# Kernel tuning notes

Hardware: AMD Instinct MI355X
Metric: run time of the kernel (lower is better)

The kernel has to match this reference:

```python
import jax, jax.numpy as jnp
import numpy as np

B, L, H = 2, 2048, 2048
NH, KVH = 16, 4
D = H // NH          # 128
G = NH // KVH        # 4 query heads per kv head
LN_EPS = 1e-12


def setup_inputs() -> dict:
    key = jax.random.key(0)
    ks = jax.random.split(key, 6)
    s = 0.02
    return {
        "hidden_state": jax.random.normal(ks[0], (B, L, H), jnp.float32),
        "mask": jnp.zeros((B, 1, 1, L), jnp.float32),
        "Wq": jax.random.normal(ks[1], (H, H), jnp.float32) * s,
        "bq": jnp.zeros((H,), jnp.float32),
        "Wk": jax.random.normal(ks[2], (KVH * D, H), jnp.float32) * s,
        "bk": jnp.zeros((KVH * D,), jnp.float32),
        "Wv": jax.random.normal(ks[3], (KVH * D, H), jnp.float32) * s,
        "bv": jnp.zeros((KVH * D,), jnp.float32),
        "Wo": jax.random.normal(ks[4], (H, H), jnp.float32) * s,
        "bo": jnp.zeros((H,), jnp.float32),
        "ln_g": jnp.ones((H,), jnp.float32),
        "ln_b": jnp.zeros((H,), jnp.float32),
    }


def _layernorm(x, g, b):
    mu = jnp.mean(x, axis=-1, keepdims=True)
    var = jnp.mean(jnp.square(x - mu), axis=-1, keepdims=True)
    return (x - mu) * jax.lax.rsqrt(var + LN_EPS) * g + b


def reference(hidden_state, mask, Wq, bq, Wk, bk, Wv, bv, Wo, bo, ln_g, ln_b):
    x = hidden_state
    # projections: b l (h d)
    q = x @ Wq.T + bq            # [B,L,NH*D]
    k = x @ Wk.T + bk            # [B,L,KVH*D]
    v = x @ Wv.T + bv            # [B,L,KVH*D]
    # b l (h d) -> b h l d, with q heads grouped per kv head (GQA broadcast,
    # mathematically identical to repeat_kv + dense SDPA)
    q = q.reshape(B, L, KVH, G, D).transpose(0, 2, 3, 1, 4)   # [B,KVH,G,L,D]
    k = k.reshape(B, L, KVH, D).transpose(0, 2, 1, 3)         # [B,KVH,L,D]
    v = v.reshape(B, L, KVH, D).transpose(0, 2, 1, 3)         # [B,KVH,L,D]
    scale = 1.0 / jnp.sqrt(jnp.float32(D))
    scores = jnp.einsum('bkgld,bkmd->bkglm', q, k) * scale    # [B,KVH,G,L,L]
    scores = scores + mask[:, :, None]                         # broadcast [B,1,1,1,L]
    attn = jax.nn.softmax(scores, axis=-1)
    out = jnp.einsum('bkglm,bkmd->bkgld', attn, v)            # [B,KVH,G,L,D]
    out = out.transpose(0, 3, 1, 2, 4).reshape(B, L, H)       # b h l d -> b l (h d)
    # SelfOutput: dense + residual + layernorm
    out = out @ Wo.T + bo
    return _layernorm(out + x, ln_g, ln_b)
```

## Files before the change

kernel.cpp:

```cpp
#include <hip/hip_runtime.h>
#include <math.h>

typedef short v8s __attribute__((ext_vector_type(8)));
typedef short v4s __attribute__((ext_vector_type(4)));
typedef float v4f __attribute__((ext_vector_type(4)));
typedef unsigned long long ull;

constexpr int L_ = 2048;
constexpr int H_ = 2048;
constexpr float LOG2E = 1.4426950408889634f;
constexpr float QSCALE = 0.08838834764831845f * LOG2E;

__device__ inline unsigned short f2bf(float f) {
    unsigned int u = __float_as_uint(f);
    u += 0x7fffu + ((u >> 16) & 1u);
    return (unsigned short)(u >> 16);
}

__device__ inline unsigned int pk2bf(float lo, float hi) {
    unsigned int a = __float_as_uint(lo) + 0x8000u;
    unsigned int b = __float_as_uint(hi) + 0x8000u;
    return __builtin_amdgcn_perm(b, a, 0x07060302);
}

__device__ inline void async16(const void* g, void* l) {
    __builtin_amdgcn_global_load_lds(
        (const __attribute__((address_space(1))) unsigned int*)g,
        (__attribute__((address_space(3))) unsigned int*)l, 16, 0, 0);
}

__global__ __launch_bounds__(256) void conv_all(
    const float* __restrict__ x,  const float* __restrict__ wq,
    const float* __restrict__ wk, const float* __restrict__ wv,
    const float* __restrict__ wo, const float* __restrict__ mask,
    unsigned short* __restrict__ xb, unsigned short* __restrict__ wqkvb,
    unsigned short* __restrict__ wob, float* __restrict__ maskL)
{
    int u = blockIdx.x * 256 + threadIdx.x;
    const float* s;
    unsigned short* d;
    if (u < 1048576)      { s = x  + (size_t)u * 8;             d = xb   + (size_t)u * 8; }
    else if (u < 1572864) { size_t t = (size_t)(u - 1048576) * 8; s = wq + t; d = wqkvb + t; }
    else if (u < 1703936) { size_t t = (size_t)(u - 1572864) * 8; s = wk + t; d = wqkvb + (size_t)2048 * 2048 + t; }
    else if (u < 1835008) { size_t t = (size_t)(u - 1703936) * 8; s = wv + t; d = wqkvb + (size_t)2560 * 2048 + t; }
    else if (u < 2359296) { size_t t = (size_t)(u - 1835008) * 8; s = wo + t; d = wob + t; }
    else if (u < 2359808) {
        int m = (u - 2359296) * 8;
        float4 a = *(const float4*)(mask + m);
        float4 b = *(const float4*)(mask + m + 4);
        float4 oa = {a.x * LOG2E, a.y * LOG2E, a.z * LOG2E, a.w * LOG2E};
        float4 ob = {b.x * LOG2E, b.y * LOG2E, b.z * LOG2E, b.w * LOG2E};
        *(float4*)(maskL + m) = oa;
        *(float4*)(maskL + m + 4) = ob;
        return;
    } else return;
    float4 a = *(const float4*)s;
    float4 b = *(const float4*)(s + 4);
    v8s o;
    o[0] = (short)f2bf(a.x); o[1] = (short)f2bf(a.y);
    o[2] = (short)f2bf(a.z); o[3] = (short)f2bf(a.w);
    o[4] = (short)f2bf(b.x); o[5] = (short)f2bf(b.y);
    o[6] = (short)f2bf(b.z); o[7] = (short)f2bf(b.w);
    *(v8s*)d = o;
}

template <int MODE>
__global__ __launch_bounds__(256) void gemm_mfma(
    const unsigned short* __restrict__ A, const unsigned short* __restrict__ W,
    const float* __restrict__ b0, const float* __restrict__ b1,
    const float* __restrict__ b2,
    unsigned short* __restrict__ oq, unsigned short* __restrict__ ok,
    unsigned short* __restrict__ ov,
    float* __restrict__ of, const float* __restrict__ resid,
    int K, int N)
{
    __shared__ short SM[3 * 8192];

    const int tid  = threadIdx.x;
    const int lane = tid & 63;
    const int wave = tid >> 6;
    const int lid  = lane & 15;
    const int g    = lane >> 4;
    const int wr   = wave >> 1, wc = wave & 1;
    const int row0 = blockIdx.y * 128, col0 = blockIdx.x * 128;

    auto stage = [&](int k0, int buf) {
#pragma unroll
        for (int i = 0; i < 2; ++i) {
            int idx = tid + i * 256;
            int r = idx >> 2, s = idx & 3;
            int c = s ^ ((r >> 1) & 3);
            async16(A + (size_t)(row0 + r) * K + k0 + c * 8,
                    &SM[buf * 8192 + idx * 8]);
            async16(W + (size_t)(col0 + r) * K + k0 + c * 8,
                    &SM[buf * 8192 + 4096 + idx * 8]);
        }
    };

    v4f acc[4][4];
#pragma unroll
    for (int i = 0; i < 4; ++i)
#pragma unroll
        for (int j = 0; j < 4; ++j) acc[i][j] = (v4f){0.f, 0.f, 0.f, 0.f};

    stage(0, 0);
    stage(32, 1);
    int p = 0;
    for (int k0 = 0; k0 < K; k0 += 32) {
        __syncthreads();
        if (k0 + 64 < K) {
            int nb = p + 2; if (nb >= 3) nb -= 3;
            stage(k0 + 64, nb);
        }
        const short* As = &SM[p * 8192];
        const short* Bs = &SM[p * 8192 + 4096];

        v8s af[4], bf[4];
#pragma unroll
        for (int t = 0; t < 4; ++t) {
            int ra = wr * 64 + t * 16 + lid;
            int rb = wc * 64 + t * 16 + lid;
            af[t] = *(const v8s*)&As[ra * 32 + ((g ^ ((ra >> 1) & 3)) * 8)];
            bf[t] = *(const v8s*)&Bs[rb * 32 + ((g ^ ((rb >> 1) & 3)) * 8)];
        }
#pragma unroll
        for (int mt = 0; mt < 4; ++mt)
#pragma unroll
            for (int nt = 0; nt < 4; ++nt)
                acc[mt][nt] = __builtin_amdgcn_mfma_f32_16x16x32_bf16(
                    af[mt], bf[nt], acc[mt][nt], 0, 0, 0);
        if (++p == 3) p = 0;
    }

    const int crow = row0 + wr * 64, ccol = col0 + wc * 64;
    if (MODE == 0) {
#pragma unroll
        for (int mt = 0; mt < 4; ++mt)
#pragma unroll
            for (int nt = 0; nt < 4; ++nt) {
                int cc = ccol + nt * 16 + lid;
                float bb = b0[cc];
#pragma unroll
                for (int r = 0; r < 4; ++r) {
                    int rr = crow + mt * 16 + g * 4 + r;
                    of[(size_t)rr * N + cc] =
                        acc[mt][nt][r] + bb + resid[(size_t)rr * N + cc];
                }
            }
    } else {
        const int seg = (col0 < 2048) ? 0 : (col0 < 2560 ? 1 : 2);
#pragma unroll
        for (int mt = 0; mt < 4; ++mt)
#pragma unroll
            for (int nt = 0; nt < 4; ++nt) {
                int cc = ccol + nt * 16 + lid;
                if (seg == 0) {
                    float bb = b0[cc];
#pragma unroll
                    for (int r = 0; r < 4; ++r) {
                        int rr = crow + mt * 16 + g * 4 + r;
                        oq[(size_t)rr * 2048 + cc] =
                            f2bf((acc[mt][nt][r] + bb) * QSCALE);
                    }
                } else if (seg == 1) {
                    float bb = b1[cc - 2048];
#pragma unroll
                    for (int r = 0; r < 4; ++r) {
                        int rr = crow + mt * 16 + g * 4 + r;
                        ok[(size_t)rr * 512 + (cc - 2048)] =
                            f2bf(acc[mt][nt][r] + bb);
                    }
                } else {
                    float bb = b2[cc - 2560];
                    int dprime = cc - 2560;
                    int colb = (crow & 2047) + ((mt >> 1) << 5) +
                               (g << 3) + ((mt & 1) << 2);
                    size_t vrow = (size_t)((crow >> 11) * 512 + dprime);
                    unsigned int lo =
                        (unsigned int)f2bf(acc[mt][nt][0] + bb) |
                        ((unsigned int)f2bf(acc[mt][nt][1] + bb) << 16);
                    unsigned int hi =
                        (unsigned int)f2bf(acc[mt][nt][2] + bb) |
                        ((unsigned int)f2bf(acc[mt][nt][3] + bb) << 16);
                    uint2 pkv; pkv.x = lo; pkv.y = hi;
                    *(uint2*)&ov[vrow * 2048 + colb] = pkv;
                }
            }
    }
}

__global__ __launch_bounds__(512) void flash_mfma(
    const unsigned short* __restrict__ Q,
    const unsigned short* __restrict__ K,
    const unsigned short* __restrict__ Vt,
    const float* __restrict__ maskL,
    unsigned short* __restrict__ AO)
{
    __shared__ short K_s[2][32 * 128];
    __shared__ short V_s[2][128 * 32];

    const int tid  = threadIdx.x;
    const int lane = tid & 63;
    const int wave = tid >> 6;
    const int lid  = lane & 15;
    const int g    = lane >> 4;
    const int lh   = (lid >> 2) & 3;

    const int c7   = blockIdx.x & 7;
    const int kvh  = c7 >> 1;
    const int b    = c7 & 1;
    const int rest = blockIdx.x >> 3;
    const int h    = kvh * 4 + (rest & 3);
    const int q0   = (rest >> 2) * 256;
    const int wq   = wave * 32;

    const unsigned short* pK;
    const unsigned short* pV;
    {
        int kr = tid >> 4, ks = tid & 15;
        pK = K + ((size_t)(b * L_ + kr)) * 512 + kvh * 128 +
             ((ks ^ (kr & 15)) * 8);
        int vd = tid >> 2, vs = tid & 3;
        pV = Vt + ((size_t)(b * 512 + kvh * 128 + vd)) * 2048 +
             ((vs ^ ((vd >> 2) & 3)) * 8);
    }

    v8s bq[2][4];
    {
        const size_t base = ((size_t)(b * L_ + q0 + wq + lid)) * 2048 + h * 128;
#pragma unroll
        for (int qt = 0; qt < 2; ++qt)
#pragma unroll
            for (int kc = 0; kc < 4; ++kc)
                bq[qt][kc] = *(const v8s*)(Q + base + (size_t)qt * 16 * 2048 +
                                           kc * 32 + g * 8);
    }

    v4f oacc[2][8];
#pragma unroll
    for (int mt = 0; mt < 2; ++mt)
#pragma unroll
        for (int nt = 0; nt < 8; ++nt) oacc[mt][nt] = (v4f){0.f, 0.f, 0.f, 0.f};
    float lsm[2] = {0.f, 0.f};

    async16(pK, &K_s[0][tid * 8]);
    async16(pV, &V_s[0][tid * 8]);

    for (int it = 0; it < 64; ++it) {
        const int p = it & 1;
        const int k0 = it * 32;
        __syncthreads();
        pK += 32 * 512;
        pV += 32;
        if (it + 1 < 64) {
            async16(pK, &K_s[p ^ 1][tid * 8]);
            async16(pV, &V_s[p ^ 1][tid * 8]);
        }
        const short* Ks = K_s[p];
        const short* Vs = V_s[p];

        v4f sacc[2][2];
#pragma unroll
        for (int kt = 0; kt < 2; ++kt) {
            float4 mk = *(const float4*)&maskL[b * L_ + k0 + kt * 16 + g * 4];
            v4f seed = {mk.x, mk.y, mk.z, mk.w};
            sacc[kt][0] = seed;
            sacc[kt][1] = seed;
        }
#pragma unroll
        for (int kc = 0; kc < 4; ++kc)
#pragma unroll
            for (int kt = 0; kt < 2; ++kt) {
                v8s ak = *(const v8s*)&Ks[(kt * 16 + lid) * 128 +
                                          (((kc * 4 + g) ^ lid) * 8)];
#pragma unroll
                for (int qt = 0; qt < 2; ++qt)
                    sacc[kt][qt] = __builtin_amdgcn_mfma_f32_16x16x32_bf16(
                        ak, bq[qt][kc], sacc[kt][qt], 0, 0, 0);
            }

        v8s ap[2];
#pragma unroll
        for (int qt = 0; qt < 2; ++qt) {
            float e0 = __builtin_amdgcn_exp2f(sacc[0][qt][0]);
            float e1 = __builtin_amdgcn_exp2f(sacc[0][qt][1]);
            float e2 = __builtin_amdgcn_exp2f(sacc[0][qt][2]);
            float e3 = __builtin_amdgcn_exp2f(sacc[0][qt][3]);
            float f0 = __builtin_amdgcn_exp2f(sacc[1][qt][0]);
            float f1 = __builtin_amdgcn_exp2f(sacc[1][qt][1]);
            float f2 = __builtin_amdgcn_exp2f(sacc[1][qt][2]);
            float f3 = __builtin_amdgcn_exp2f(sacc[1][qt][3]);
            lsm[qt] += ((e0 + e1) + (e2 + e3)) + ((f0 + f1) + (f2 + f3));
            union { uint4 u; v8s v; } pa;
            pa.u.x = pk2bf(e0, e1);
            pa.u.y = pk2bf(e2, e3);
            pa.u.z = pk2bf(f0, f1);
            pa.u.w = pk2bf(f2, f3);
            ap[qt] = pa.v;
        }

#pragma unroll
        for (int nt = 0; nt < 8; ++nt) {
            v8s bv = *(const v8s*)&Vs[(nt * 16 + lid) * 32 + ((g ^ lh) * 8)];
#pragma unroll
            for (int mt = 0; mt < 2; ++mt)
                oacc[mt][nt] = __builtin_amdgcn_mfma_f32_16x16x32_bf16(
                    ap[mt], bv, oacc[mt][nt], 0, 0, 0);
        }
    }

#pragma unroll
    for (int qt = 0; qt < 2; ++qt) {
        lsm[qt] += __shfl_xor(lsm[qt], 16);
        lsm[qt] += __shfl_xor(lsm[qt], 32);
    }
#pragma unroll
    for (int mt = 0; mt < 2; ++mt) {
        float linv[4];
#pragma unroll
        for (int r = 0; r < 4; ++r) linv[r] = 1.0f / __shfl(lsm[mt], g * 4 + r);
#pragma unroll
        for (int nt = 0; nt < 8; ++nt)
#pragma unroll
            for (int r = 0; r < 4; ++r) {
                size_t orow = (size_t)(b * L_ + q0 + wq + mt * 16 + g * 4 + r);
                AO[orow * 2048 + h * 128 + nt * 16 + lid] =
                    f2bf(oacc[mt][nt][r] * linv[r]);
            }
    }
}

__global__ __launch_bounds__(256) void ln_kernel(
    const float* __restrict__ P, const float* __restrict__ g,
    const float* __restrict__ bta, float* __restrict__ Out)
{
    const int row = blockIdx.x;
    const int tid = threadIdx.x;
    const float* p = P + (size_t)row * H_;

    float vals[8];
    float s = 0.f;
#pragma unroll
    for (int it = 0; it < 2; ++it) {
        int c = tid * 4 + it * 1024;
        float4 a = *(const float4*)&p[c];
        vals[it * 4 + 0] = a.x; vals[it * 4 + 1] = a.y;
        vals[it * 4 + 2] = a.z; vals[it * 4 + 3] = a.w;
        s += a.x + a.y + a.z + a.w;
    }
    __shared__ float red[4];
    float t = s;
#pragma unroll
    for (int off = 32; off > 0; off >>= 1) t += __shfl_xor(t, off);
    if ((tid & 63) == 0) red[tid >> 6] = t;
    __syncthreads();
    float mean = (red[0] + red[1] + red[2] + red[3]) * (1.f / (float)H_);

    float vsum = 0.f;
#pragma unroll
    for (int i = 0; i < 8; ++i) {
        float d = vals[i] - mean;
        vsum += d * d;
    }
    __syncthreads();
    t = vsum;
#pragma unroll
    for (int off = 32; off > 0; off >>= 1) t += __shfl_xor(t, off);
    if ((tid & 63) == 0) red[tid >> 6] = t;
    __syncthreads();
    float var = (red[0] + red[1] + red[2] + red[3]) * (1.f / (float)H_);
    float rs  = 1.f / sqrtf(var + 1e-12f);

#pragma unroll
    for (int it = 0; it < 2; ++it) {
        int c = tid * 4 + it * 1024;
        float4 gv = *(const float4*)&g[c];
        float4 bv = *(const float4*)&bta[c];
        float4 ov;
        ov.x = (vals[it * 4 + 0] - mean) * rs * gv.x + bv.x;
        ov.y = (vals[it * 4 + 1] - mean) * rs * gv.y + bv.y;
        ov.z = (vals[it * 4 + 2] - mean) * rs * gv.z + bv.z;
        ov.w = (vals[it * 4 + 3] - mean) * rs * gv.w + bv.w;
        *(float4*)&Out[(size_t)row * H_ + c] = ov;
    }
}

extern "C" void kernel_launch(void* const* d_in, const int* in_sizes, int n_in,
                              void* d_out, int out_size, void* d_ws, size_t ws_size,
                              hipStream_t stream)
{
    const float* x    = (const float*)d_in[0];
    const float* mask = (const float*)d_in[1];
    const float* Wq   = (const float*)d_in[2];
    const float* bq   = (const float*)d_in[3];
    const float* Wk   = (const float*)d_in[4];
    const float* bk   = (const float*)d_in[5];
    const float* Wv   = (const float*)d_in[6];
    const float* bv   = (const float*)d_in[7];
    const float* Wo   = (const float*)d_in[8];
    const float* bo   = (const float*)d_in[9];
    const float* lng  = (const float*)d_in[10];
    const float* lnb  = (const float*)d_in[11];
    float* out = (float*)d_out;

    char* ws = (char*)d_ws;
    unsigned short* xb    = (unsigned short*)(ws);
    unsigned short* wqkv  = (unsigned short*)(ws + 16777216);
    float*          maskL = (float*)         (ws + 29360128);
    unsigned short* q     = (unsigned short*)(ws + 29376512);
    unsigned short* k     = (unsigned short*)(ws + 46153728);
    unsigned short* vt    = (unsigned short*)(ws + 54542336);
    unsigned short* ao    = (unsigned short*)(ws + 58736640);
    unsigned short* wob   = (unsigned short*)(ws + 75513856);
    float*          pj    = (float*)(ws);

    dim3 blk(256);
    conv_all<<<9218, blk, 0, stream>>>(x, Wq, Wk, Wv, Wo, mask,
                                       xb, wqkv, wob, maskL);

    gemm_mfma<3><<<dim3(24, 32), blk, 0, stream>>>(
        xb, wqkv, bq, bk, bv, q, k, vt, nullptr, nullptr, 2048, 3072);

    flash_mfma<<<dim3(256), dim3(512), 0, stream>>>(q, k, vt, maskL, ao);

    gemm_mfma<0><<<dim3(16, 32), blk, 0, stream>>>(
        ao, wob, bo, nullptr, nullptr, nullptr, nullptr, nullptr, pj, x, 2048, 2048);
    ln_kernel<<<4096, blk, 0, stream>>>(pj, lng, lnb, out);
}
```

Before: 343.0 us.

## Software-pipeline flash attention so PV of previous tile overlaps next QK

Restructures the attention inner loop so that, at each step, the QK^T MFMAs for tile t are issued alongside the PV MFMAs for tile t-1, with the softmax exponentials done after both. This aims to hide the exp/convert latency behind matrix work. V shared memory grows to a triple buffer so the tile still in use for PV is not overwritten by the async prefetch. The cost is more LDS and more live registers (sacc and ap held across stages), which may reduce occupancy or cause spills.

New measurement: 344.8 us. No clear change (+0.5%).

```diff
diff --git a/kernel.cpp b/kernel.cpp
--- a/kernel.cpp
+++ b/kernel.cpp
@@ -197,7 +197,7 @@
     unsigned short* __restrict__ AO)
 {
     __shared__ short K_s[2][32 * 128];
-    __shared__ short V_s[2][128 * 32];
+    __shared__ short V_s[3][128 * 32];
 
     const int tid  = threadIdx.x;
     const int lane = tid & 63;
@@ -213,6 +213,8 @@
     const int h    = kvh * 4 + (rest & 3);
     const int q0   = (rest >> 2) * 256;
     const int wq   = wave * 32;
+
+    const float* mb = maskL + b * L_;
 
     const unsigned short* pK;
     const unsigned short* pV;
@@ -242,27 +244,13 @@
 #pragma unroll
         for (int nt = 0; nt < 8; ++nt) oacc[mt][nt] = (v4f){0.f, 0.f, 0.f, 0.f};
     float lsm[2] = {0.f, 0.f};
-
-    async16(pK, &K_s[0][tid * 8]);
-    async16(pV, &V_s[0][tid * 8]);
-
-    for (int it = 0; it < 64; ++it) {
-        const int p = it & 1;
-        const int k0 = it * 32;
-        __syncthreads();
-        pK += 32 * 512;
-        pV += 32;
-        if (it + 1 < 64) {
-            async16(pK, &K_s[p ^ 1][tid * 8]);
-            async16(pV, &V_s[p ^ 1][tid * 8]);
-        }
-        const short* Ks = K_s[p];
-        const short* Vs = V_s[p];
-
-        v4f sacc[2][2];
+    v4f sacc[2][2];
+    v8s ap[2];
+
+    auto qk = [&](int k0, const short* Ks) {
 #pragma unroll
         for (int kt = 0; kt < 2; ++kt) {
-            float4 mk = *(const float4*)&maskL[b * L_ + k0 + kt * 16 + g * 4];
+            float4 mk = *(const float4*)&mb[k0 + kt * 16 + g * 4];
             v4f seed = {mk.x, mk.y, mk.z, mk.w};
             sacc[kt][0] = seed;
             sacc[kt][1] = seed;
@@ -278,8 +266,20 @@
                     sacc[kt][qt] = __builtin_amdgcn_mfma_f32_16x16x32_bf16(
                         ak, bq[qt][kc], sacc[kt][qt], 0, 0, 0);
             }
-
-        v8s ap[2];
+    };
+
+    auto pv = [&](const short* Vs) {
+#pragma unroll
+        for (int nt = 0; nt < 8; ++nt) {
+            v8s bv = *(const v8s*)&Vs[(nt * 16 + lid) * 32 + ((g ^ lh) * 8)];
+#pragma unroll
+            for (int mt = 0; mt < 2; ++mt)
+                oacc[mt][nt] = __builtin_amdgcn_mfma_f32_16x16x32_bf16(
+                    ap[mt], bv, oacc[mt][nt], 0, 0, 0);
+        }
+    };
+
+    auto sm = [&]() {
 #pragma unroll
         for (int qt = 0; qt < 2; ++qt) {
             float e0 = __builtin_amdgcn_exp2f(sacc[0][qt][0]);
@@ -298,16 +298,31 @@
             pa.u.w = pk2bf(f2, f3);
             ap[qt] = pa.v;
         }
-
-#pragma unroll
-        for (int nt = 0; nt < 8; ++nt) {
-            v8s bv = *(const v8s*)&Vs[(nt * 16 + lid) * 32 + ((g ^ lh) * 8)];
-#pragma unroll
-            for (int mt = 0; mt < 2; ++mt)
-                oacc[mt][nt] = __builtin_amdgcn_mfma_f32_16x16x32_bf16(
-                    ap[mt], bv, oacc[mt][nt], 0, 0, 0);
-        }
-    }
+    };
+
+    async16(pK, &K_s[0][tid * 8]);
+    async16(pV, &V_s[0][tid * 8]);
+    __syncthreads();
+    pK += 32 * 512; pV += 32;
+    async16(pK, &K_s[1][tid * 8]);
+    async16(pV, &V_s[1][tid * 8]);
+    qk(0, K_s[0]);
+    sm();
+
+    int vprev = 0;
+    for (int t = 1; t < 64; ++t) {
+        __syncthreads();
+        if (t + 1 < 64) {
+            pK += 32 * 512; pV += 32;
+            async16(pK, &K_s[(t + 1) & 1][tid * 8]);
+            async16(pV, &V_s[(t + 1) % 3][tid * 8]);
+        }
+        qk(t * 32, K_s[t & 1]);
+        pv(V_s[vprev]);
+        sm();
+        if (++vprev == 3) vprev = 0;
+    }
+    pv(V_s[0]);
 
 #pragma unroll
     for (int qt = 0; qt < 2; ++qt) {
```
